# Kernel optimization log

Measured on AMD Instinct MI355X. Metric: run time of the kernel, lower is better.

Reference implementation:

```python
import jax, jax.numpy as jnp
import numpy as np

V, E, S, TT, H, C, B = 50000, 300, 128, 12, 512, 3, 128


def setup_inputs() -> dict:
    key = jax.random.key(0)
    ks = jax.random.split(key, 12)
    sc = lambda n: 1.0 / np.sqrt(n)
    return {
        "target_ids": jax.random.randint(ks[0], (B, TT), 0, V),
        "target_len": jax.random.randint(ks[1], (B,), 1, TT + 1, dtype=jnp.int32),
        "left_ids": jax.random.randint(ks[2], (B, S), 0, V),
        "left_len": jax.random.randint(ks[3], (B,), 1, S + 1, dtype=jnp.int32),
        "right_ids": jax.random.randint(ks[4], (B, S), 0, V),
        "right_len": jax.random.randint(ks[5], (B,), 1, S + 1, dtype=jnp.int32),
        "embeddings": jax.random.normal(ks[6], (V, E), jnp.float32) * 0.1,
        "W_left": jax.random.normal(ks[7], (2 * E + H, 4 * H), jnp.float32) * sc(2 * E + H),
        "b_left": jnp.zeros((4 * H,), jnp.float32),
        "W_right": jax.random.normal(ks[8], (2 * E + H, 4 * H), jnp.float32) * sc(2 * E + H),
        "b_right": jnp.zeros((4 * H,), jnp.float32),
        "W_dense": jax.random.normal(ks[9], (2 * H, C), jnp.float32) * sc(2 * H),
        "b_dense": jnp.zeros((C,), jnp.float32),
    }


def _lstm_last_state(x, lens, W, b):
    # x: [B,S,D] inputs, lens: [B]; TF BasicLSTMCell gate order (i, j, f, o), forget_bias=1.0.
    # dynamic_rnn(sequence_length=lens): state frozen once t >= len.
    b_, s_, _ = x.shape
    xs = jnp.swapaxes(x, 0, 1)  # [S,B,D]
    step_mask = jnp.arange(s_)[:, None] < lens[None, :]  # [S,B]
    h0 = jnp.zeros((b_, H), x.dtype)
    c0 = jnp.zeros((b_, H), x.dtype)

    def step(carry, inp):
        h, c = carry
        x_t, m_t = inp
        z = jnp.concatenate([x_t, h], axis=-1) @ W + b  # [B,4H]
        i, j, f, o = jnp.split(z, 4, axis=-1)
        c_new = jax.nn.sigmoid(f + 1.0) * c + jax.nn.sigmoid(i) * jnp.tanh(j)
        h_new = jax.nn.sigmoid(o) * jnp.tanh(c_new)
        m = m_t[:, None]
        return (jnp.where(m, h_new, h), jnp.where(m, c_new, c)), None

    (h, _c), _ = jax.lax.scan(step, (h0, c0), (xs, step_mask))
    return h


def reference(target_ids, target_len, left_ids, left_len, right_ids, right_len,
              embeddings, W_left, b_left, W_right, b_right, W_dense, b_dense):
    # mean target embedding over valid target tokens (variable_len_batch_mean)
    tgt = embeddings[target_ids]  # [B,TT,E]
    tmask = (jnp.arange(TT)[None, :] < target_len[:, None]).astype(tgt.dtype)
    mean_t = jnp.sum(tgt * tmask[:, :, None], axis=1) / target_len[:, None].astype(tgt.dtype)  # [B,E]

    def ctx_inputs(ids):
        e = embeddings[ids]  # [B,S,E]
        # stack([emb, mean_t], axis=2) then reshape -> per-timestep concat [emb_t, mean_t]
        return jnp.concatenate([e, jnp.broadcast_to(mean_t[:, None, :], e.shape)], axis=-1)  # [B,S,2E]

    h_l = _lstm_last_state(ctx_inputs(left_ids), left_len, W_left, b_left)
    h_r = _lstm_last_state(ctx_inputs(right_ids), right_len, W_right, b_right)
    logits = jnp.concatenate([h_l, h_r], axis=-1) @ W_dense + b_dense  # [B,C]
    return logits
```

## Files before the change

kernel.cpp:

```cpp
#include <hip/hip_runtime.h>

#define NB 128
#define NS 128
#define NT 12
#define NE 300
#define NH 512
#define NCOL 2048
#define WGSC __HIP_MEMORY_SCOPE_WORKGROUP

typedef _Float16 h8v __attribute__((ext_vector_type(8)));
typedef __attribute__((ext_vector_type(4))) float f4v;
typedef __attribute__((ext_vector_type(4))) int   i4v;

__device__ __forceinline__ unsigned short f2h(float f) {
  union { _Float16 h; unsigned short u; } c; c.h = (_Float16)f; return c.u;
}
__device__ __forceinline__ float sigm(float x) { return 1.f / (1.f + __expf(-x)); }
__device__ __forceinline__ float tanh_(float x) { const float e = __expf(2.f * x); return 1.f - 2.f / (e + 1.f); }

__device__ __forceinline__ void st32f_uc(float* p, float v) {
  asm volatile("global_store_dword %0, %1, off sc1" :: "v"(p), "v"(v) : "memory");
}
__device__ __forceinline__ void st32i_uc(int* p, int v) {
  asm volatile("global_store_dword %0, %1, off sc1" :: "v"(p), "v"(v) : "memory");
}
__device__ __forceinline__ int ldflag(const int* p) {
  int v;
  asm volatile("global_load_dword %0, %1, off sc1\n\ts_waitcnt vmcnt(0)" : "=v"(v) : "v"(p) : "memory");
  return v;
}
__device__ __forceinline__ void ld4_uc(const char* a, i4v* r) {
  asm volatile(
    "global_load_dwordx4 %0, %4, off sc1\n\t"
    "global_load_dwordx4 %1, %4, off offset:256 sc1\n\t"
    "global_load_dwordx4 %2, %4, off offset:512 sc1\n\t"
    "global_load_dwordx4 %3, %4, off offset:768 sc1\n\t"
    "s_waitcnt vmcnt(0)"
    : "=&v"(r[0]), "=&v"(r[1]), "=&v"(r[2]), "=&v"(r[3])
    : "v"(a) : "memory");
}

struct Params {
  const int *tids, *tlen, *lids, *llen, *rids, *rlen;
  const float *emb, *Wl, *bl, *Wr, *br, *Wd, *bd;
  float* out;
  unsigned short* hbuf;
  float* hfin;
  int* bar;
};

__device__ __forceinline__ void lspin(int* c, int tgt) {
  while (__hip_atomic_load(c, __ATOMIC_RELAXED, WGSC) < tgt) {}
  __builtin_amdgcn_fence(__ATOMIC_ACQUIRE, "workgroup");
}
__device__ __forceinline__ void larrive(int* c) {
  __hip_atomic_fetch_add(c, 1, __ATOMIC_ACQ_REL, WGSC);
}

#define OFF_HS   0
#define OFF_XS   16384
#define OFF_ZX   26624
#define OFF_ZS   51200
#define OFF_HOUT 59392
#define OFF_WTH  51200
#define OFF_WTX  34816
#define LDS_SZ   61440

__global__ __launch_bounds__(512, 1) void lstm_all(Params p) {
  __shared__ __align__(16) char lds[LDS_SZ];
  __shared__ int lenL[16];
  __shared__ float redL[8][4];
  __shared__ int cnt[8];

  const int tid = threadIdx.x;
  const int wid = blockIdx.x;
  if (tid < 8) cnt[tid] = 0;

  const int g = wid & 15, ht = wid >> 4;
  const int side = g & 1, bt = g >> 1;
  const int b0 = bt * 16, d0c = ht * 32;
  const int* lenp = side ? p.rlen : p.llen;
  const int* gids = side ? p.rids : p.lids;
  const float* W = side ? p.Wr : p.Wl;
  const float* bias = side ? p.br : p.bl;
  int* fl = p.bar + g * 1024;

  const bool isH = tid < 256;
  const int wv = tid >> 6;
  const int ln = tid & 63;
  const int lwv = isH ? wv : (wv - 4);
  const int kgrp = ln >> 4;
  const int stid = tid & 255;

  float* meanTT = (float*)lds;
  float* zS = (float*)(lds + OFF_ZS);

  {
    const int r = tid >> 5, l32 = tid & 31;
    const int b = b0 + r;
    const int Lt = p.tlen[b];
    const float inv = 1.f / (float)Lt;
    int toks[NT];
    #pragma unroll
    for (int t = 0; t < NT; ++t) toks[t] = p.tids[b * NT + t];
    for (int k = l32; k < NE; k += 32) {
      float s = 0.f;
      #pragma unroll
      for (int t = 0; t < NT; ++t)
        if (t < Lt) s += p.emb[(size_t)toks[t] * NE + k];
      meanTT[k * 16 + r] = s * inv;
    }
    if (tid < 16) lenL[tid] = lenp[b0 + tid];
  }
  __syncthreads();

  if (isH) {
    const int row_c = stid >> 4;
    const int dloc = stid & 15;

    float zb1[4], zb2[4];
    {
      #pragma unroll
      for (int gq = 0; gq < 4; ++gq) {
        const float* wp = W + (size_t)NE * NCOL + gq * NH + d0c;
        float a1 = bias[gq * NH + d0c + dloc];
        float a2 = bias[gq * NH + d0c + dloc + 16];
        for (int k = 0; k < NE; ++k) {
          const float m = meanTT[k * 16 + row_c];
          a1 += m * wp[(size_t)k * NCOL + dloc];
          a2 += m * wp[(size_t)k * NCOL + dloc + 16];
        }
        zb1[gq] = a1; zb2[gq] = a2;
      }
    }
    if (ln == 0) larrive(&cnt[6]);

    int he = 0;
    auto hpbar = [&]() {
      ++he;
      if (ln == 0) larrive(&cnt[7]);
      while (__hip_atomic_load(&cnt[7], __ATOMIC_RELAXED, WGSC) < 4 * he) {}
      __builtin_amdgcn_fence(__ATOMIC_ACQUIRE, "workgroup");
    };
    h8v hfr0[16], hfr1[16];
    {
      unsigned short* wT = (unsigned short*)(lds + OFF_WTH);
      const int r3 = stid >> 3;
      const int part = stid & 7;
      const int gate_p = part >> 1, half_p = part & 1;
      for (int i = 0; i < 16; ++i) {
        const int k = 600 + i * 32 + r3;
        const float* wr = W + (size_t)k * NCOL + gate_p * NH + d0c + half_p * 16;
        const f4v a0 = *(const f4v*)wr;
        const f4v a1 = *(const f4v*)(wr + 4);
        const f4v a2 = *(const f4v*)(wr + 8);
        const f4v a3 = *(const f4v*)(wr + 12);
        #pragma unroll
        for (int j = 0; j < 4; ++j) {
          wT[(part * 16 + j) * 32 + r3]      = f2h(a0[j]);
          wT[(part * 16 + 4 + j) * 32 + r3]  = f2h(a1[j]);
          wT[(part * 16 + 8 + j) * 32 + r3]  = f2h(a2[j]);
          wT[(part * 16 + 12 + j) * 32 + r3] = f2h(a3[j]);
        }
        hpbar();
        const int c0 = lwv * 32 + (ln & 15);
        hfr0[i] = *(const h8v*)((char*)wT + c0 * 64 + kgrp * 16);
        hfr1[i] = *(const h8v*)((char*)wT + (c0 + 16) * 64 + kgrp * 16);
        hpbar();
      }
    }

    float cR1 = 0.f, cR2 = 0.f, hR1 = 0.f, hR2 = 0.f;
    const int a_r = ln & 15;
    const int srow = lwv * 4 + (ln >> 4);
    for (int t = 0; t < NS; ++t) {
      lspin(&cnt[2], 4 * (t + 1));
      const float* zx = (const float*)(lds + OFF_ZX + (t % 3) * 8192);
      f4v acc0, acc1;
      #pragma unroll
      for (int rg = 0; rg < 4; ++rg) {
        const int rr = kgrp * 4 + rg;
        acc0[rg] = zx[rr * 128 + lwv * 32 + (ln & 15)];
        acc1[rg] = zx[rr * 128 + lwv * 32 + 16 + (ln & 15)];
      }
      if (ln == 0) larrive(&cnt[3]);

      if (t) {
        {
          int v = 1 << 30;
          const int* f = fl + (ln & 15);
          if (ln < 16) v = ldflag(f);
          while (__ballot(v < t) != 0ull) { if (ln < 16) v = ldflag(f); }
        }
        const char* src = (const char*)(p.hbuf
            + (size_t)(((t & 1) * 2 + side) * NB + b0 + srow) * NH) + (ln & 15) * 16;
        i4v hv[4];
        ld4_uc(src, hv);
        #pragma unroll
        for (int q = 0; q < 4; ++q) {
          const int c16 = (ln & 15) + 16 * q;
          *(i4v*)(lds + OFF_HS + srow * 1024 + ((c16 * 16) ^ ((srow & 7) << 4))) = hv[q];
        }
        if (ln == 0) larrive(&cnt[0]);
        while (__hip_atomic_load(&cnt[0], __ATOMIC_RELAXED, WGSC) < 4 * t) {}
        __builtin_amdgcn_fence(__ATOMIC_ACQUIRE, "workgroup");
        #pragma unroll
        for (int kt = 0; kt < 16; ++kt) {
          h8v a = *(const h8v*)(lds + OFF_HS + a_r * 1024
                                + (((kt * 4 + kgrp) * 16) ^ ((a_r & 7) << 4)));
          acc0 = __builtin_amdgcn_mfma_f32_16x16x32_f16(a, hfr0[kt], acc0, 0, 0, 0);
          acc1 = __builtin_amdgcn_mfma_f32_16x16x32_f16(a, hfr1[kt], acc1, 0, 0, 0);
        }
      }

      #pragma unroll
      for (int rg = 0; rg < 4; ++rg) {
        const int rr = kgrp * 4 + rg;
        zS[rr * 128 + lwv * 32 + (ln & 15)]      = acc0[rg];
        zS[rr * 128 + lwv * 32 + 16 + (ln & 15)] = acc1[rg];
      }
      if (ln == 0) larrive(&cnt[4]);
      while (__hip_atomic_load(&cnt[4], __ATOMIC_RELAXED, WGSC) < 4 * (t + 1)) {}
      __builtin_amdgcn_fence(__ATOMIC_ACQUIRE, "workgroup");

      {
        unsigned short* hOut = (unsigned short*)(lds + OFF_HOUT + (t & 1) * 1024);
        const float* zr = zS + row_c * 128;
        float zi = zr[0 * 32 + dloc] + zb1[0], zj = zr[1 * 32 + dloc] + zb1[1];
        float zf = zr[2 * 32 + dloc] + zb1[2], zo = zr[3 * 32 + dloc] + zb1[3];
        float ig = sigm(zi), jg = tanh_(zj), fg = sigm(zf + 1.f), og = sigm(zo);
        float cn = fg * cR1 + ig * jg;
        float hn = og * tanh_(cn);
        if (t < lenL[row_c]) { cR1 = cn; hR1 = hn; }
        hOut[row_c * 32 + dloc] = f2h(hR1);
        zi = zr[0 * 32 + dloc + 16] + zb2[0]; zj = zr[1 * 32 + dloc + 16] + zb2[1];
        zf = zr[2 * 32 + dloc + 16] + zb2[2]; zo = zr[3 * 32 + dloc + 16] + zb2[3];
        ig = sigm(zi); jg = tanh_(zj); fg = sigm(zf + 1.f); og = sigm(zo);
        cn = fg * cR2 + ig * jg; hn = og * tanh_(cn);
        if (t < lenL[row_c]) { cR2 = cn; hR2 = hn; }
        hOut[row_c * 32 + dloc + 16] = f2h(hR2);
      }

      if (ln == 0) larrive(&cnt[5]);
      if (lwv == (t & 3)) {
        while (__hip_atomic_load(&cnt[5], __ATOMIC_RELAXED, WGSC) < 4 * (t + 1)) {}
        __builtin_amdgcn_fence(__ATOMIC_ACQUIRE, "workgroup");
        const int prow = ln >> 2, ppart = ln & 3;
        i4v hv = *(const i4v*)(lds + OFF_HOUT + (t & 1) * 1024 + prow * 64 + ppart * 16);
        unsigned short* dst = p.hbuf
            + (size_t)((((t + 1) & 1) * 2 + side) * NB + b0 + prow) * NH + d0c + ppart * 8;
        asm volatile("global_store_dwordx4 %0, %1, off sc1\n\ts_waitcnt vmcnt(0)"
                     :: "v"(dst), "v"(hv) : "memory");
        if (ln == 0) st32i_uc(fl + ht, t + 1);
      }
    }

    st32f_uc(&p.hfin[((size_t)side * NB + b0 + row_c) * NH + d0c + dloc], hR1);
    st32f_uc(&p.hfin[((size_t)side * NB + b0 + row_c) * NH + d0c + dloc + 16], hR2);
    asm volatile("s_waitcnt vmcnt(0)" ::: "memory");
    if (ln == 0) larrive(&cnt[5]);
    if (lwv == 0) {
      while (__hip_atomic_load(&cnt[5], __ATOMIC_RELAXED, WGSC) < 4 * NS + 4) {}
      if (ln == 0) st32i_uc(fl + ht, NS + 1);
    }
  } else {
    int xe = 0;
    auto xbar = [&]() {
      ++xe;
      if (ln == 0) larrive(&cnt[1]);
      while (__hip_atomic_load(&cnt[1], __ATOMIC_RELAXED, WGSC) < 4 * xe) {}
      __builtin_amdgcn_fence(__ATOMIC_ACQUIRE, "workgroup");
    };

    h8v xfr0[10], xfr1[10];
    {
      unsigned short* wT = (unsigned short*)(lds + OFF_WTX);
      const int r3 = stid >> 3, part = stid & 7;
      const int gate_p = part >> 1, half_p = part & 1;
      for (int i = 0; i < 10; ++i) {
        const int k = i * 32 + r3;
        float v[16];
        if (k < NE) {
          const float* wr = W + (size_t)k * NCOL + gate_p * NH + d0c + half_p * 16;
          const f4v a0 = *(const f4v*)wr;
          const f4v a1 = *(const f4v*)(wr + 4);
          const f4v a2 = *(const f4v*)(wr + 8);
          const f4v a3 = *(const f4v*)(wr + 12);
          #pragma unroll
          for (int j = 0; j < 4; ++j) {
            v[j] = a0[j]; v[4 + j] = a1[j]; v[8 + j] = a2[j]; v[12 + j] = a3[j];
          }
        } else {
          #pragma unroll
          for (int j = 0; j < 16; ++j) v[j] = 0.f;
        }
        #pragma unroll
        for (int j = 0; j < 16; ++j)
          wT[(part * 16 + j) * 32 + r3] = f2h(v[j]);
        xbar();
        const int c0 = lwv * 32 + (ln & 15);
        xfr0[i] = *(const h8v*)((char*)wT + c0 * 64 + kgrp * 16);
        xfr1[i] = *(const h8v*)((char*)wT + (c0 + 16) * 64 + kgrp * 16);
        xbar();
      }
    }

    lspin(&cnt[6], 4);

    for (int n = 0; n < NS; ++n) {
      if (n >= 3) lspin(&cnt[3], 4 * (n - 2));
      {
        const int xrow = stid >> 4;
        const int tok = gids[(size_t)(b0 + xrow) * NS + n];
        const float* ep_ = p.emb + (size_t)tok * NE;
        #pragma unroll
        for (int j = 0; j < 3; ++j) {
          const int c16 = (stid & 15) + j * 16;
          if (c16 < 40) {
            unsigned short tmp[8];
            if (c16 < 37) {
              const f4v v0 = *(const f4v*)(ep_ + c16 * 8);
              const f4v v1 = *(const f4v*)(ep_ + c16 * 8 + 4);
              tmp[0] = f2h(v0[0]); tmp[1] = f2h(v0[1]); tmp[2] = f2h(v0[2]); tmp[3] = f2h(v0[3]);
              tmp[4] = f2h(v1[0]); tmp[5] = f2h(v1[1]); tmp[6] = f2h(v1[2]); tmp[7] = f2h(v1[3]);
            } else if (c16 == 37) {
              const f4v v0 = *(const f4v*)(ep_ + 296);
              tmp[0] = f2h(v0[0]); tmp[1] = f2h(v0[1]); tmp[2] = f2h(v0[2]); tmp[3] = f2h(v0[3]);
              tmp[4] = 0; tmp[5] = 0; tmp[6] = 0; tmp[7] = 0;
            } else {
              #pragma unroll
              for (int q = 0; q < 8; ++q) tmp[q] = 0;
            }
            *(i4v*)(lds + OFF_XS + xrow * 640 + ((c16 * 16) ^ ((xrow & 7) << 4))) = *(const i4v*)tmp;
          }
        }
      }
      xbar();
      f4v a0 = {0.f, 0.f, 0.f, 0.f}, a1 = {0.f, 0.f, 0.f, 0.f};
      const int a_r = ln & 15;
      #pragma unroll
      for (int kt = 0; kt < 10; ++kt) {
        h8v a = *(const h8v*)(lds + OFF_XS + a_r * 640
                              + (((kt * 4 + kgrp) * 16) ^ ((a_r & 7) << 4)));
        a0 = __builtin_amdgcn_mfma_f32_16x16x32_f16(a, xfr0[kt], a0, 0, 0, 0);
        a1 = __builtin_amdgcn_mfma_f32_16x16x32_f16(a, xfr1[kt], a1, 0, 0, 0);
      }
      float* zx = (float*)(lds + OFF_ZX + (n % 3) * 8192);
      #pragma unroll
      for (int rg = 0; rg < 4; ++rg) {
        const int rr = kgrp * 4 + rg;
        zx[rr * 128 + lwv * 32 + (ln & 15)]      = a0[rg];
        zx[rr * 128 + lwv * 32 + 16 + (ln & 15)] = a1[rg];
      }
      if (ln == 0) larrive(&cnt[2]);
      xbar();
    }
  }

  if (wid < NB) {
    const int b = wid, bth = b >> 4;
    if (tid < 32) {
      const int gh = (bth << 1) + (tid >> 4);
      const int* f = p.bar + gh * 1024 + (tid & 15);
      int v = ldflag(f);
      while (__ballot(v < NS + 1) != 0ull) { __builtin_amdgcn_s_sleep(2); v = ldflag(f); }
    }
    __syncthreads();

    float a0 = 0.f, a1 = 0.f, a2 = 0.f;
    #pragma unroll
    for (int q = 0; q < 2; ++q) {
      const int kk = q * 512 + tid;
      const int hs = kk >> 9, dim = kk & 511;
      const float* hp = &p.hfin[((size_t)hs * NB + b) * NH + dim];
      const float hv = __hip_atomic_load(hp, __ATOMIC_RELAXED, __HIP_MEMORY_SCOPE_AGENT);
      a0 += hv * p.Wd[kk * 3 + 0];
      a1 += hv * p.Wd[kk * 3 + 1];
      a2 += hv * p.Wd[kk * 3 + 2];
    }
    #pragma unroll
    for (int s = 32; s > 0; s >>= 1) {
      a0 += __shfl_down(a0, s, 64);
      a1 += __shfl_down(a1, s, 64);
      a2 += __shfl_down(a2, s, 64);
    }
    if (ln == 0) { redL[wv][0] = a0; redL[wv][1] = a1; redL[wv][2] = a2; }
    __syncthreads();
    if (tid == 0) {
      float o0 = p.bd[0], o1 = p.bd[1], o2 = p.bd[2];
      #pragma unroll
      for (int w = 0; w < 8; ++w) { o0 += redL[w][0]; o1 += redL[w][1]; o2 += redL[w][2]; }
      p.out[b * 3 + 0] = o0;
      p.out[b * 3 + 1] = o1;
      p.out[b * 3 + 2] = o2;
    }
  }
}

extern "C" void kernel_launch(void* const* d_in, const int* in_sizes, int n_in,
                              void* d_out, int out_size, void* d_ws, size_t ws_size,
                              hipStream_t stream) {
  (void)in_sizes; (void)n_in; (void)out_size; (void)ws_size;
  char* ws = (char*)d_ws;
  Params p;
  p.tids = (const int*)d_in[0];
  p.tlen = (const int*)d_in[1];
  p.lids = (const int*)d_in[2];
  p.llen = (const int*)d_in[3];
  p.rids = (const int*)d_in[4];
  p.rlen = (const int*)d_in[5];
  p.emb  = (const float*)d_in[6];
  p.Wl   = (const float*)d_in[7];
  p.bl   = (const float*)d_in[8];
  p.Wr   = (const float*)d_in[9];
  p.br   = (const float*)d_in[10];
  p.Wd   = (const float*)d_in[11];
  p.bd   = (const float*)d_in[12];
  p.out  = (float*)d_out;
  p.bar  = (int*)ws;
  p.hbuf = (unsigned short*)(ws + 65536);
  p.hfin = (float*)(ws + 65536 + 524288);
  hipMemsetAsync(ws, 0, 65536, stream);
  lstm_all<<<dim3(256), dim3(512), 0, stream>>>(p);
}
```

Measured before the change: 488.7 us.

## Replace per-step flag handshake with tag bits embedded in fp16 hidden state

Each thread now writes its two fp16 hidden values straight to the global exchange buffer as one packed dword. The low mantissa bit of each half carries a step-parity tag. Consumers spin-load the 64-byte row chunk until every tag matches the expected step, which removes the separate flag store/poll, the LDS staging buffer and one workgroup barrier per timestep. In exchange, the fp16 h loses its least significant mantissa bit. The whole hbuf is now zeroed each launch, and the spin loop re-reads full chunks rather than a single flag.

```diff
diff --git a/kernel.cpp b/kernel.cpp
--- a/kernel.cpp
+++ b/kernel.cpp
@@ -18,10 +18,20 @@
 __device__ __forceinline__ float sigm(float x) { return 1.f / (1.f + __expf(-x)); }
 __device__ __forceinline__ float tanh_(float x) { const float e = __expf(2.f * x); return 1.f - 2.f / (e + 1.f); }
 
+__device__ __forceinline__ unsigned packh(float a, float b, int tag) {
+  unsigned lo = f2h(a), hi = f2h(b);
+  lo = (lo & ~1u) | (unsigned)(tag & 1);
+  hi = (hi & ~1u) | (unsigned)((tag >> 1) & 1);
+  return lo | (hi << 16);
+}
+
 __device__ __forceinline__ void st32f_uc(float* p, float v) {
   asm volatile("global_store_dword %0, %1, off sc1" :: "v"(p), "v"(v) : "memory");
 }
 __device__ __forceinline__ void st32i_uc(int* p, int v) {
+  asm volatile("global_store_dword %0, %1, off sc1" :: "v"(p), "v"(v) : "memory");
+}
+__device__ __forceinline__ void st32u_uc(unsigned* p, unsigned v) {
   asm volatile("global_store_dword %0, %1, off sc1" :: "v"(p), "v"(v) : "memory");
 }
 __device__ __forceinline__ int ldflag(const int* p) {
@@ -29,12 +39,12 @@
   asm volatile("global_load_dword %0, %1, off sc1\n\ts_waitcnt vmcnt(0)" : "=v"(v) : "v"(p) : "memory");
   return v;
 }
-__device__ __forceinline__ void ld4_uc(const char* a, i4v* r) {
+__device__ __forceinline__ void ld64_uc(const char* a, i4v* r) {
   asm volatile(
     "global_load_dwordx4 %0, %4, off sc1\n\t"
-    "global_load_dwordx4 %1, %4, off offset:256 sc1\n\t"
-    "global_load_dwordx4 %2, %4, off offset:512 sc1\n\t"
-    "global_load_dwordx4 %3, %4, off offset:768 sc1\n\t"
+    "global_load_dwordx4 %1, %4, off offset:16 sc1\n\t"
+    "global_load_dwordx4 %2, %4, off offset:32 sc1\n\t"
+    "global_load_dwordx4 %3, %4, off offset:48 sc1\n\t"
     "s_waitcnt vmcnt(0)"
     : "=&v"(r[0]), "=&v"(r[1]), "=&v"(r[2]), "=&v"(r[3])
     : "v"(a) : "memory");
@@ -61,10 +71,9 @@
 #define OFF_XS   16384
 #define OFF_ZX   26624
 #define OFF_ZS   51200
-#define OFF_HOUT 59392
 #define OFF_WTH  51200
 #define OFF_WTX  34816
-#define LDS_SZ   61440
+#define LDS_SZ   59392
 
 __global__ __launch_bounds__(512, 1) void lstm_all(Params p) {
   __shared__ __align__(16) char lds[LDS_SZ];
@@ -116,19 +125,19 @@
 
   if (isH) {
     const int row_c = stid >> 4;
-    const int dloc = stid & 15;
+    const int m = stid & 15;
 
     float zb1[4], zb2[4];
     {
       #pragma unroll
       for (int gq = 0; gq < 4; ++gq) {
         const float* wp = W + (size_t)NE * NCOL + gq * NH + d0c;
-        float a1 = bias[gq * NH + d0c + dloc];
-        float a2 = bias[gq * NH + d0c + dloc + 16];
+        float a1 = bias[gq * NH + d0c + 2 * m];
+        float a2 = bias[gq * NH + d0c + 2 * m + 1];
         for (int k = 0; k < NE; ++k) {
-          const float m = meanTT[k * 16 + row_c];
-          a1 += m * wp[(size_t)k * NCOL + dloc];
-          a2 += m * wp[(size_t)k * NCOL + dloc + 16];
+          const float mv = meanTT[k * 16 + row_c];
+          a1 += mv * wp[(size_t)k * NCOL + 2 * m];
+          a2 += mv * wp[(size_t)k * NCOL + 2 * m + 1];
         }
         zb1[gq] = a1; zb2[gq] = a2;
       }
@@ -172,7 +181,8 @@
 
     float cR1 = 0.f, cR2 = 0.f, hR1 = 0.f, hR2 = 0.f;
     const int a_r = ln & 15;
-    const int srow = lwv * 4 + (ln >> 4);
+    const int srow = stid >> 4;
+    const int schk = stid & 15;
     for (int t = 0; t < NS; ++t) {
       lspin(&cnt[2], 4 * (t + 1));
       const float* zx = (const float*)(lds + OFF_ZX + (t % 3) * 8192);
@@ -186,20 +196,24 @@
       if (ln == 0) larrive(&cnt[3]);
 
       if (t) {
-        {
-          int v = 1 << 30;
-          const int* f = fl + (ln & 15);
-          if (ln < 16) v = ldflag(f);
-          while (__ballot(v < t) != 0ull) { if (ln < 16) v = ldflag(f); }
-        }
         const char* src = (const char*)(p.hbuf
-            + (size_t)(((t & 1) * 2 + side) * NB + b0 + srow) * NH) + (ln & 15) * 16;
-        i4v hv[4];
-        ld4_uc(src, hv);
+            + (size_t)(((t & 1) * 2 + side) * NB + b0 + srow) * NH + schk * 32);
+        const unsigned exp32 = ((unsigned)(t & 1)) | (((unsigned)((t >> 1) & 1)) << 16);
+        i4v v[4];
+        for (;;) {
+          ld64_uc(src, v);
+          unsigned bad = 0;
+          #pragma unroll
+          for (int q = 0; q < 4; ++q)
+            #pragma unroll
+            for (int j = 0; j < 4; ++j)
+              bad |= (((unsigned)v[q][j]) ^ exp32) & 0x00010001u;
+          if (!bad) break;
+        }
         #pragma unroll
         for (int q = 0; q < 4; ++q) {
-          const int c16 = (ln & 15) + 16 * q;
-          *(i4v*)(lds + OFF_HS + srow * 1024 + ((c16 * 16) ^ ((srow & 7) << 4))) = hv[q];
+          const int c16 = schk * 4 + q;
+          *(i4v*)(lds + OFF_HS + srow * 1024 + ((c16 * 16) ^ ((srow & 7) << 4))) = v[q];
         }
         if (ln == 0) larrive(&cnt[0]);
         while (__hip_atomic_load(&cnt[0], __ATOMIC_RELAXED, WGSC) < 4 * t) {}
@@ -224,43 +238,31 @@
       __builtin_amdgcn_fence(__ATOMIC_ACQUIRE, "workgroup");
 
       {
-        unsigned short* hOut = (unsigned short*)(lds + OFF_HOUT + (t & 1) * 1024);
         const float* zr = zS + row_c * 128;
-        float zi = zr[0 * 32 + dloc] + zb1[0], zj = zr[1 * 32 + dloc] + zb1[1];
-        float zf = zr[2 * 32 + dloc] + zb1[2], zo = zr[3 * 32 + dloc] + zb1[3];
+        float zi = zr[0 * 32 + 2 * m] + zb1[0], zj = zr[1 * 32 + 2 * m] + zb1[1];
+        float zf = zr[2 * 32 + 2 * m] + zb1[2], zo = zr[3 * 32 + 2 * m] + zb1[3];
         float ig = sigm(zi), jg = tanh_(zj), fg = sigm(zf + 1.f), og = sigm(zo);
         float cn = fg * cR1 + ig * jg;
         float hn = og * tanh_(cn);
         if (t < lenL[row_c]) { cR1 = cn; hR1 = hn; }
-        hOut[row_c * 32 + dloc] = f2h(hR1);
-        zi = zr[0 * 32 + dloc + 16] + zb2[0]; zj = zr[1 * 32 + dloc + 16] + zb2[1];
-        zf = zr[2 * 32 + dloc + 16] + zb2[2]; zo = zr[3 * 32 + dloc + 16] + zb2[3];
+        zi = zr[0 * 32 + 2 * m + 1] + zb2[0]; zj = zr[1 * 32 + 2 * m + 1] + zb2[1];
+        zf = zr[2 * 32 + 2 * m + 1] + zb2[2]; zo = zr[3 * 32 + 2 * m + 1] + zb2[3];
         ig = sigm(zi); jg = tanh_(zj); fg = sigm(zf + 1.f); og = sigm(zo);
         cn = fg * cR2 + ig * jg; hn = og * tanh_(cn);
         if (t < lenL[row_c]) { cR2 = cn; hR2 = hn; }
-        hOut[row_c * 32 + dloc + 16] = f2h(hR2);
-      }
-
-      if (ln == 0) larrive(&cnt[5]);
-      if (lwv == (t & 3)) {
-        while (__hip_atomic_load(&cnt[5], __ATOMIC_RELAXED, WGSC) < 4 * (t + 1)) {}
-        __builtin_amdgcn_fence(__ATOMIC_ACQUIRE, "workgroup");
-        const int prow = ln >> 2, ppart = ln & 3;
-        i4v hv = *(const i4v*)(lds + OFF_HOUT + (t & 1) * 1024 + prow * 64 + ppart * 16);
-        unsigned short* dst = p.hbuf
-            + (size_t)((((t + 1) & 1) * 2 + side) * NB + b0 + prow) * NH + d0c + ppart * 8;
-        asm volatile("global_store_dwordx4 %0, %1, off sc1\n\ts_waitcnt vmcnt(0)"
-                     :: "v"(dst), "v"(hv) : "memory");
-        if (ln == 0) st32i_uc(fl + ht, t + 1);
-      }
-    }
-
-    st32f_uc(&p.hfin[((size_t)side * NB + b0 + row_c) * NH + d0c + dloc], hR1);
-    st32f_uc(&p.hfin[((size_t)side * NB + b0 + row_c) * NH + d0c + dloc + 16], hR2);
+        unsigned pk = packh(hR1, hR2, (t + 1) & 3);
+        unsigned* dst = (unsigned*)p.hbuf
+            + ((size_t)((((t + 1) & 1) * 2 + side) * NB + b0 + row_c) * (NH / 2)) + d0c / 2 + m;
+        st32u_uc(dst, pk);
+      }
+    }
+
+    st32f_uc(&p.hfin[((size_t)side * NB + b0 + row_c) * NH + d0c + 2 * m], hR1);
+    st32f_uc(&p.hfin[((size_t)side * NB + b0 + row_c) * NH + d0c + 2 * m + 1], hR2);
     asm volatile("s_waitcnt vmcnt(0)" ::: "memory");
     if (ln == 0) larrive(&cnt[5]);
     if (lwv == 0) {
-      while (__hip_atomic_load(&cnt[5], __ATOMIC_RELAXED, WGSC) < 4 * NS + 4) {}
+      while (__hip_atomic_load(&cnt[5], __ATOMIC_RELAXED, WGSC) < 4) {}
       if (ln == 0) st32i_uc(fl + ht, NS + 1);
     }
   } else {
@@ -420,6 +422,6 @@
   p.bar  = (int*)ws;
   p.hbuf = (unsigned short*)(ws + 65536);
   p.hfin = (float*)(ws + 65536 + 524288);
-  hipMemsetAsync(ws, 0, 65536, stream);
+  hipMemsetAsync(ws, 0, 65536 + 524288, stream);
   lstm_all<<<dim3(256), dim3(512), 0, stream>>>(p);
 }
```

After: 435.1 us. 11.0% less time.
